# Kernel optimization log

Hardware: AMD Instinct MI355X
Metric: run time of the kernel (lower is better)

## Reference

```python
import jax, jax.numpy as jnp
import numpy as np
from jax import lax

B, H, W = 8, 64, 64
C = 192          # in_channel == out_channel
CI = 384         # inner_channel = int(2.0 * C)


def setup_inputs() -> dict:
    key = jax.random.key(0)
    ks = jax.random.split(key, 8)
    s = 0.02
    return {
        "x": jax.random.normal(ks[0], (B, H, W, C), jnp.float32),
        "Win": jax.random.normal(ks[1], (C, 2 * CI), jnp.float32) * s,
        "conv_w": jax.random.normal(ks[2], (CI, 1, 3, 3), jnp.float32) * s,
        "conv_b": jnp.zeros((CI,), jnp.float32),
        "Wout": jax.random.normal(ks[3], (CI, C), jnp.float32) * s,
        "Wm1": jax.random.normal(ks[4], (C, 4 * C), jnp.float32) * s,
        "bm1": jnp.zeros((4 * C,), jnp.float32),
        "Wm2": jax.random.normal(ks[5], (4 * C, C), jnp.float32) * s,
        "bm2": jnp.zeros((C,), jnp.float32),
    }


def reference(x, Win, conv_w, conv_b, Wout, Wm1, bm1, Wm2, bm2):
    silu = jax.nn.silu
    shortcut = x                                   # [B,H,W,C], norm1 is Identity (norm=None)
    xz = jnp.einsum('bhwc,cd->bhwd', x, Win)       # in_proj (no bias) -> [B,H,W,2*CI]
    x1, z = jnp.split(xz, 2, axis=-1)
    # channel_recover -> [B,CI,H,W], depthwise conv + silu
    xc = jnp.transpose(x1, (0, 3, 1, 2))
    xc = lax.conv_general_dilated(xc, conv_w, (1, 1), 'SAME',
                                  feature_group_count=CI,
                                  dimension_numbers=('NCHW', 'OIHW', 'NCHW'))
    xc = silu(xc + conv_b[None, :, None, None])
    L = H * W
    # cross_scan: K=2 views (row-major and transposed), doubled by flip_scan -> [B,4,CI,L]
    x0 = xc.reshape(B, CI, L)
    xt = jnp.transpose(xc, (0, 1, 3, 2)).reshape(B, CI, L)
    x_cross = jnp.stack([x0, xt], axis=1)
    xs = jnp.concatenate([x_cross, jnp.flip(x_cross, axis=-1)], axis=1)
    out_y = xs  # ssm() is abstract in MBaseBlock -> identity passthrough
    # scan_proj (CrossMerge): undo flips and permutations, sum branches
    inv_y = jnp.flip(out_y[:, 2:4], axis=-1)

    def unperm(v):  # branch scanned in transposed (W,H) order -> back to (H,W)
        return jnp.transpose(v.reshape(B, CI, W, H), (0, 1, 3, 2)).reshape(B, CI, L)

    y = out_y[:, 0] + inv_y[:, 0] + unperm(out_y[:, 1]) + unperm(inv_y[:, 1])
    y = jnp.transpose(y, (0, 2, 1)).reshape(B, H, W, CI)  # norm2 is Identity
    y = y * silu(z)                                       # gate
    out = jnp.einsum('bhwc,cd->bhwd', y, Wout)            # out_proj (no bias)
    out = shortcut + out                                  # dropout/drop_path are Identity
    # dense is Identity (in_channel == out_channel); MLP branch 192->768->192
    h = silu(jnp.einsum('bhwc,cd->bhwd', out, Wm1) + bm1)
    mlp = jnp.einsum('bhwd,dc->bhwc', h, Wm2) + bm2
    return out + mlp
```

## Files before the change

kernel.cpp:

```cpp
#include <hip/hip_runtime.h>
#include <hip/hip_bf16.h>

#define BDIM 8
#define HDIM 64
#define WDIM 64
#define CDIM 192
#define CIDIM 384
#define MTOK (BDIM * HDIM * WDIM)

using bf16 = __hip_bfloat16;
typedef __attribute__((ext_vector_type(8))) short short8;
typedef __attribute__((ext_vector_type(4))) float f32x4;

__device__ __forceinline__ float silu_f(float v) { return v / (1.0f + __expf(-v)); }
__device__ __forceinline__ float bf2f(short s) {
    union { unsigned u; float f; } x; x.u = ((unsigned)(unsigned short)s) << 16; return x.f;
}

__device__ __forceinline__ void gload_lds16(const bf16* g, bf16* l) {
    __builtin_amdgcn_global_load_lds(
        (const __attribute__((address_space(1))) void*)g,
        (__attribute__((address_space(3))) void*)l, 16, 0, 0);
}

#define MFMA16(a, b, c) __builtin_amdgcn_mfma_f32_16x16x32_bf16(a, b, c, 0, 0, 0)

#define NSTRIPE 40
template <int EPI>
__launch_bounds__(256, 2)
__global__ void gemm_k192_p(const bf16* __restrict__ A, const bf16* __restrict__ BT,
                            const float* __restrict__ bias,
                            bf16* __restrict__ outB, bf16* __restrict__ outB2)
{
    __shared__ bf16 As[2][64 * 192];
    __shared__ bf16 Bs[64 * 192];

    const int bid = blockIdx.x;
    const int n   = bid / NSTRIPE;
    const int s   = bid % NSTRIPE;
    const int n0  = n * 64;

    const int tid  = threadIdx.x;
    const int lane = tid & 63;
    const int wv   = tid >> 6;
    const int wm   = wv >> 1;
    const int wn   = wv & 1;

    int soff[6];
    #pragma unroll
    for (int i = 0; i < 6; ++i) {
        const int ci   = wv * 6 + i;
        const int c    = ci * 64 + lane;
        const int row  = c / 24;
        const int slot = c - row * 24;
        soff[i] = row * 192 + (slot ^ (row & 7)) * 8;
    }

    #pragma unroll
    for (int i = 0; i < 6; ++i)
        gload_lds16(BT + (size_t)n0 * 192 + soff[i], &Bs[(wv * 6 + i) * 512]);
    #pragma unroll
    for (int i = 0; i < 6; ++i)
        gload_lds16(A + (size_t)(s * 64) * 192 + soff[i], &As[0][(wv * 6 + i) * 512]);

    const int mloc[2] = { wm * 32 + (lane & 15), wm * 32 + 16 + (lane & 15) };
    const int nloc[2] = { wn * 32 + (lane & 15), wn * 32 + 16 + (lane & 15) };
    const bool isZ = (EPI == 0) && (n0 >= CIDIM);
    bf16* dst        = (EPI == 0) ? (isZ ? outB2 : outB) : outB;
    const int stride = (EPI == 0) ? CIDIM : 768;
    const int col0   = (EPI == 0) ? (isZ ? n0 - CIDIM : n0) : n0;

    int cur = 0;
    for (int mt = s; mt < 512; mt += NSTRIPE) {
        const int nmt = mt + NSTRIPE;
        if (nmt < 512) {
            const bf16* a1 = A + (size_t)(nmt * 64) * 192;
            bf16* db = As[cur ^ 1];
            #pragma unroll
            for (int i = 0; i < 6; ++i)
                gload_lds16(a1 + soff[i], &db[(wv * 6 + i) * 512]);
            asm volatile("s_waitcnt vmcnt(6)" ::: "memory");
        } else {
            asm volatile("s_waitcnt vmcnt(0)" ::: "memory");
        }
        __builtin_amdgcn_sched_barrier(0);
        __builtin_amdgcn_s_barrier();
        __builtin_amdgcn_sched_barrier(0);

        const bf16* la = As[cur];
        f32x4 acc[2][2] = {};
        __builtin_amdgcn_s_setprio(1);
        #pragma unroll
        for (int ks = 0; ks < 6; ++ks) {
            const int t = ks * 4 + (lane >> 4);
            short8 af[2], bfr[2];
            #pragma unroll
            for (int mi = 0; mi < 2; ++mi) {
                const int m = mloc[mi];
                af[mi] = *reinterpret_cast<const short8*>(&la[m * 192 + ((t ^ (m & 7)) << 3)]);
            }
            #pragma unroll
            for (int ni = 0; ni < 2; ++ni) {
                const int nn = nloc[ni];
                bfr[ni] = *reinterpret_cast<const short8*>(&Bs[nn * 192 + ((t ^ (nn & 7)) << 3)]);
            }
            #pragma unroll
            for (int mi = 0; mi < 2; ++mi)
                #pragma unroll
                for (int ni = 0; ni < 2; ++ni)
                    acc[mi][ni] = MFMA16(af[mi], bfr[ni], acc[mi][ni]);
        }
        __builtin_amdgcn_s_setprio(0);

        __builtin_amdgcn_sched_barrier(0);
        __builtin_amdgcn_s_barrier();
        __builtin_amdgcn_sched_barrier(0);

        const int m0   = mt * 64;
        const int rowb = m0 + wm * 32 + (lane >> 4) * 4;
        const int colb = col0 + wn * 32 + (lane & 15);
        #pragma unroll
        for (int mi = 0; mi < 2; ++mi) {
            #pragma unroll
            for (int ni = 0; ni < 2; ++ni) {
                const int c = colb + ni * 16;
                #pragma unroll
                for (int j = 0; j < 4; ++j) {
                    const int row = rowb + mi * 16 + j;
                    float v = acc[mi][ni][j];
                    if constexpr (EPI == 0) {
                        if (isZ) v = 4.0f * silu_f(v);
                    } else {
                        v = silu_f(v + bias[n0 + (c - col0)]);
                    }
                    dst[(size_t)row * stride + c] = __float2bfloat16(v);
                }
            }
        }
        cur ^= 1;
    }
}

__launch_bounds__(256, 4)
__global__ void gemm_g3(const bf16* __restrict__ A, const bf16* __restrict__ BT,
                        const bf16* __restrict__ residB, bf16* __restrict__ outB,
                        int M, int N, int K, int NX)
{
    __shared__ bf16 As[128 * 64];
    __shared__ bf16 Bs[64 * 64];

    const int bid = blockIdx.x;
    const int c8  = bid & 7;
    const int kq  = bid >> 3;
    const int bx  = kq % NX;
    const int by  = (kq / NX) * 8 + c8;
    const int m0  = by * 128;
    const int n0  = bx * 64;

    const int tid  = threadIdx.x;
    const int lane = tid & 63;
    const int wv   = tid >> 6;
    const int wm   = wv >> 1;
    const int wn   = wv & 1;

    const int srow  = lane >> 3;
    const int sslot = lane & 7;

    f32x4 acc[4][2] = {};

    for (int k0 = 0; k0 < K; k0 += 64) {
        #pragma unroll
        for (int i = 0; i < 4; ++i) {
            const int rb = wv * 32 + i * 8;
            const int r  = rb + srow;
            gload_lds16(A + (size_t)(m0 + r) * K + k0 + ((sslot ^ (r & 7)) << 3),
                        &As[rb * 64]);
        }
        #pragma unroll
        for (int i = 0; i < 2; ++i) {
            const int rb = wv * 16 + i * 8;
            const int r  = rb + srow;
            gload_lds16(BT + (size_t)(n0 + r) * K + k0 + ((sslot ^ (r & 7)) << 3),
                        &Bs[rb * 64]);
        }
        __syncthreads();

        #pragma unroll
        for (int kk = 0; kk < 2; ++kk) {
            const int t = kk * 4 + (lane >> 4);
            short8 af[4], bfr[2];
            #pragma unroll
            for (int mi = 0; mi < 4; ++mi) {
                const int m = wm * 64 + mi * 16 + (lane & 15);
                af[mi] = *reinterpret_cast<const short8*>(&As[m * 64 + ((t ^ (m & 7)) << 3)]);
            }
            #pragma unroll
            for (int ni = 0; ni < 2; ++ni) {
                const int n = wn * 32 + ni * 16 + (lane & 15);
                bfr[ni] = *reinterpret_cast<const short8*>(&Bs[n * 64 + ((t ^ (n & 7)) << 3)]);
            }
            #pragma unroll
            for (int mi = 0; mi < 4; ++mi)
                #pragma unroll
                for (int ni = 0; ni < 2; ++ni)
                    acc[mi][ni] = MFMA16(af[mi], bfr[ni], acc[mi][ni]);
        }
        __syncthreads();
    }

    const int colb = n0 + wn * 32 + (lane & 15);
    const int rowb = m0 + wm * 64 + (lane >> 4) * 4;
    #pragma unroll
    for (int mi = 0; mi < 4; ++mi) {
        #pragma unroll
        for (int ni = 0; ni < 2; ++ni) {
            const int c = colb + ni * 16;
            #pragma unroll
            for (int j = 0; j < 4; ++j) {
                const int row = rowb + mi * 16 + j;
                const size_t off = (size_t)row * N + c;
                outB[off] = __float2bfloat16(acc[mi][ni][j] +
                                             bf2f(*(const short*)&residB[off]));
            }
        }
    }
}

#define HSTR 776
__launch_bounds__(256, 2)
__global__ void fused_mlp32(const bf16* __restrict__ ob, const bf16* __restrict__ Wm1F,
                            const bf16* __restrict__ Wm2F, const float* __restrict__ bm1,
                            const float* __restrict__ bm2, float* __restrict__ out)
{
    __shared__ bf16 obs[32 * 192];
    __shared__ bf16 hs[32 * HSTR];

    const int m0   = blockIdx.x * 32;
    const int tid  = threadIdx.x;
    const int lane = tid & 63;
    const int wv   = tid >> 6;
    const int l15  = lane & 15;
    const int l4   = lane >> 4;

    #pragma unroll
    for (int i = 0; i < 3; ++i) {
        const int ci   = wv * 3 + i;
        const int c    = ci * 64 + lane;
        const int row  = c / 24;
        const int slot = c - row * 24;
        gload_lds16(ob + (size_t)(m0 + row) * 192 + ((slot ^ (row & 7)) << 3),
                    &obs[ci * 512]);
    }
    __syncthreads();

    #pragma unroll
    for (int g = 0; g < 3; ++g) {
        f32x4 hacc[2][4] = {};
        #pragma unroll
        for (int ks = 0; ks < 6; ++ks) {
            short8 af[2];
            #pragma unroll
            for (int mi = 0; mi < 2; ++mi) {
                const int r = mi * 16 + l15;
                af[mi] = *reinterpret_cast<const short8*>(
                    &obs[r * 192 + (((ks * 4 + l4) ^ (r & 7)) << 3)]);
            }
            #pragma unroll
            for (int ni = 0; ni < 4; ++ni) {
                const int f = wv * 12 + g * 4 + ni;
                const short8 b = *reinterpret_cast<const short8*>(
                    Wm1F + ((size_t)(f * 6 + ks) * 64 + lane) * 8);
                #pragma unroll
                for (int mi = 0; mi < 2; ++mi)
                    hacc[mi][ni] = MFMA16(af[mi], b, hacc[mi][ni]);
            }
        }
        #pragma unroll
        for (int ni = 0; ni < 4; ++ni) {
            const int col = (wv * 12 + g * 4 + ni) * 16 + l15;
            const float bb = bm1[col];
            #pragma unroll
            for (int mi = 0; mi < 2; ++mi)
                #pragma unroll
                for (int j = 0; j < 4; ++j) {
                    const int r = mi * 16 + l4 * 4 + j;
                    hs[r * HSTR + col] = __float2bfloat16(silu_f(hacc[mi][ni][j] + bb));
                }
        }
    }
    __syncthreads();

    f32x4 facc[2][3] = {};
    for (int ks = 0; ks < 24; ++ks) {
        short8 ha[2];
        #pragma unroll
        for (int mi = 0; mi < 2; ++mi) {
            const int r = mi * 16 + l15;
            ha[mi] = *reinterpret_cast<const short8*>(&hs[r * HSTR + ks * 32 + l4 * 8]);
        }
        #pragma unroll
        for (int ni = 0; ni < 3; ++ni) {
            const int f = wv * 3 + ni;
            const short8 b = *reinterpret_cast<const short8*>(
                Wm2F + ((size_t)(f * 24 + ks) * 64 + lane) * 8);
            #pragma unroll
            for (int mi = 0; mi < 2; ++mi)
                facc[mi][ni] = MFMA16(ha[mi], b, facc[mi][ni]);
        }
    }

    #pragma unroll
    for (int ni = 0; ni < 3; ++ni) {
        const int col = (wv * 3 + ni) * 16 + l15;
        const float b2 = bm2[col];
        #pragma unroll
        for (int mi = 0; mi < 2; ++mi)
            #pragma unroll
            for (int j = 0; j < 4; ++j) {
                const int r  = mi * 16 + l4 * 4 + j;
                const int ch = (col >> 3) ^ (r & 7);
                const float resid = bf2f(*reinterpret_cast<const short*>(
                    &obs[r * 192 + ch * 8 + (col & 7)]));
                out[(size_t)(m0 + r) * 192 + col] = facc[mi][ni][j] + b2 + resid;
            }
    }
}

__launch_bounds__(256)
__global__ void dwconv_gate_v6(const bf16* __restrict__ x1, const bf16* __restrict__ sz,
                               const float* __restrict__ wT, const float* __restrict__ conv_b,
                               bf16* __restrict__ y)
{
    const int bid = blockIdx.x;
    const int swz = (bid & 7) * ((int)gridDim.x >> 3) + (bid >> 3);
    const int f   = swz * 256 + threadIdx.x;
    const int m   = f / 48;
    const int cg  = f - m * 48;
    const int c0  = cg * 8;
    const int h   = (m >> 6) & 63;
    const int w   = m & 63;

    float acc[8];
    {
        const f32x4 ba = *reinterpret_cast<const f32x4*>(&conv_b[c0]);
        const f32x4 bb = *reinterpret_cast<const f32x4*>(&conv_b[c0 + 4]);
        acc[0] = ba[0]; acc[1] = ba[1]; acc[2] = ba[2]; acc[3] = ba[3];
        acc[4] = bb[0]; acc[5] = bb[1]; acc[6] = bb[2]; acc[7] = bb[3];
    }

    #pragma unroll
    for (int r = 0; r < 3; ++r) {
        const int hh = h + r - 1;
        if (hh < 0 || hh >= HDIM) continue;
        #pragma unroll
        for (int dw = 0; dw < 3; ++dw) {
            const int ww = w + dw - 1;
            if (ww < 0 || ww >= WDIM) continue;
            const int mm  = m + (r - 1) * WDIM + (dw - 1);
            const int tap = r * 3 + dw;
            const short8 t = *reinterpret_cast<const short8*>(&x1[(size_t)mm * CIDIM + c0]);
            const f32x4 wa = *reinterpret_cast<const f32x4*>(&wT[tap * CIDIM + c0]);
            const f32x4 wb = *reinterpret_cast<const f32x4*>(&wT[tap * CIDIM + c0 + 4]);
            acc[0] += bf2f(t[0]) * wa[0]; acc[1] += bf2f(t[1]) * wa[1];
            acc[2] += bf2f(t[2]) * wa[2]; acc[3] += bf2f(t[3]) * wa[3];
            acc[4] += bf2f(t[4]) * wb[0]; acc[5] += bf2f(t[5]) * wb[1];
            acc[6] += bf2f(t[6]) * wb[2]; acc[7] += bf2f(t[7]) * wb[3];
        }
    }

    const short8 g = *reinterpret_cast<const short8*>(&sz[(size_t)m * CIDIM + c0]);
    bf16 tmp[8];
    #pragma unroll
    for (int j = 0; j < 8; ++j)
        tmp[j] = __float2bfloat16(silu_f(acc[j]) * bf2f(g[j]));
    *reinterpret_cast<short8*>(&y[(size_t)m * CIDIM + c0]) =
        *reinterpret_cast<const short8*>(tmp);
}

#define SZ_WIN  (192 * 768)
#define SZ_WOUT (384 * 192)
#define SZ_WM1  (192 * 768)
#define SZ_WM2  (768 * 192)
#define SZ_CW   (CIDIM * 9)
#define XCVT    (MTOK * CDIM / 4)
#define SZ_ALL  (XCVT + SZ_WIN + SZ_WOUT + SZ_WM1 + SZ_WM2 + SZ_CW)

__launch_bounds__(256)
__global__ void prep_all(const float* __restrict__ x, const float* __restrict__ Win,
                         const float* __restrict__ Wout, const float* __restrict__ Wm1,
                         const float* __restrict__ Wm2, const float* __restrict__ convw,
                         bf16* __restrict__ xb, bf16* __restrict__ WinT,
                         bf16* __restrict__ WoutT, bf16* __restrict__ Wm1F,
                         bf16* __restrict__ Wm2F, float* __restrict__ wTc)
{
    int idx = blockIdx.x * 256 + threadIdx.x;
    if (idx < XCVT) {
        const int i = idx * 4;
        const float4 v = *reinterpret_cast<const float4*>(&x[i]);
        xb[i + 0] = __float2bfloat16(v.x);
        xb[i + 1] = __float2bfloat16(v.y);
        xb[i + 2] = __float2bfloat16(v.z);
        xb[i + 3] = __float2bfloat16(v.w);
        return;
    }
    idx -= XCVT;
    if (idx < SZ_WIN) {
        const int r = idx / 768, c = idx % 768;
        WinT[(size_t)c * 192 + r] = __float2bfloat16(Win[idx]);
        return;
    }
    idx -= SZ_WIN;
    if (idx < SZ_WOUT) {
        const int r = idx / 192, c = idx % 192;
        WoutT[(size_t)c * 384 + r] = __float2bfloat16(Wout[idx]);
        return;
    }
    idx -= SZ_WOUT;
    if (idx < SZ_WM1) {
        const int f  = idx / 3072;
        const int r1 = idx - f * 3072;
        const int ks = r1 / 512;
        const int r2 = r1 - ks * 512;
        const int l  = r2 >> 3;
        const int e  = r2 & 7;
        const int row = f * 16 + (l & 15);
        const int k   = ks * 32 + (l >> 4) * 8 + e;
        Wm1F[idx] = __float2bfloat16(Wm1[(size_t)k * 768 + row]);
        return;
    }
    idx -= SZ_WM1;
    if (idx < SZ_WM2) {
        const int f  = idx / 12288;
        const int r1 = idx - f * 12288;
        const int ks = r1 / 512;
        const int r2 = r1 - ks * 512;
        const int l  = r2 >> 3;
        const int e  = r2 & 7;
        const int row = f * 16 + (l & 15);
        const int k   = ks * 32 + (l >> 4) * 8 + e;
        Wm2F[idx] = __float2bfloat16(Wm2[(size_t)k * 192 + row]);
        return;
    }
    idx -= SZ_WM2;
    if (idx < SZ_CW) {
        const int ci = idx / 9, t = idx % 9;
        wTc[t * CIDIM + ci] = convw[idx];
    }
}

extern "C" void kernel_launch(void* const* d_in, const int* in_sizes, int n_in,
                              void* d_out, int out_size, void* d_ws, size_t ws_size,
                              hipStream_t stream)
{
    const float* x      = (const float*)d_in[0];
    const float* Win    = (const float*)d_in[1];
    const float* conv_w = (const float*)d_in[2];
    const float* conv_b = (const float*)d_in[3];
    const float* Wout   = (const float*)d_in[4];
    const float* Wm1    = (const float*)d_in[5];
    const float* bm1    = (const float*)d_in[6];
    const float* Wm2    = (const float*)d_in[7];
    const float* bm2    = (const float*)d_in[8];
    float* out = (float*)d_out;

    char* ws = (char*)d_ws;
    size_t o = 0;
    bf16*  xb    = (bf16*)(ws + o); o += (size_t)MTOK * CDIM * 2;
    bf16*  WinT  = (bf16*)(ws + o); o += (size_t)768 * 192 * 2;
    bf16*  WoutT = (bf16*)(ws + o); o += (size_t)192 * 384 * 2;
    bf16*  Wm1F  = (bf16*)(ws + o); o += (size_t)SZ_WM1 * 2;
    bf16*  Wm2F  = (bf16*)(ws + o); o += (size_t)SZ_WM2 * 2;
    float* wTc   = (float*)(ws + o); o += (size_t)9 * CIDIM * 4;
    bf16*  ws_x1 = (bf16*)(ws + o); o += (size_t)MTOK * CIDIM * 2;
    bf16*  ws_sz = (bf16*)(ws + o); o += (size_t)MTOK * CIDIM * 2;
    bf16*  ws_y  = (bf16*)(ws + o); o += (size_t)MTOK * CIDIM * 2;
    bf16*  ws_ob = (bf16*)(ws + o); o += (size_t)MTOK * CDIM * 2;

    prep_all<<<dim3((SZ_ALL + 255) / 256), dim3(256), 0, stream>>>(
        x, Win, Wout, Wm1, Wm2, conv_w, xb, WinT, WoutT, Wm1F, Wm2F, wTc);

    gemm_k192_p<0><<<dim3(12 * NSTRIPE), dim3(256), 0, stream>>>(
        xb, WinT, nullptr, ws_x1, ws_sz);

    dwconv_gate_v6<<<dim3(MTOK * 48 / 256), dim3(256), 0, stream>>>(
        ws_x1, ws_sz, wTc, conv_b, ws_y);

    gemm_g3<<<dim3(3 * 256), dim3(256), 0, stream>>>(
        ws_y, WoutT, xb, ws_ob, MTOK, CDIM, CIDIM, 3);

    fused_mlp32<<<dim3(MTOK / 32), dim3(256), 0, stream>>>(
        ws_ob, Wm1F, Wm2F, bm1, bm2, out);
}
```

Baseline: 117.1 us.

## Chunk MLP hidden dimension to shrink LDS and raise occupancy

The fused MLP kernel now computes the 768-wide hidden activation in three 256-wide chunks and accumulates the second GEMM after each chunk, instead of materialising the full hidden tile in shared memory. This cuts the hidden LDS buffer to about a third, and the launch bound is raised from 2 to 4 blocks per SM to get more resident blocks and better latency hiding. The cost is extra __syncthreads per chunk and a non-unrolled outer loop, and register pressure may limit the occupancy gain.

```diff
diff --git a/kernel.cpp b/kernel.cpp
--- a/kernel.cpp
+++ b/kernel.cpp
@@ -226,14 +226,14 @@
     }
 }
 
-#define HSTR 776
-__launch_bounds__(256, 2)
-__global__ void fused_mlp32(const bf16* __restrict__ ob, const bf16* __restrict__ Wm1F,
-                            const bf16* __restrict__ Wm2F, const float* __restrict__ bm1,
-                            const float* __restrict__ bm2, float* __restrict__ out)
+#define HST2 264
+__launch_bounds__(256, 4)
+__global__ void fused_mlp_kc(const bf16* __restrict__ ob, const bf16* __restrict__ Wm1F,
+                             const bf16* __restrict__ Wm2F, const float* __restrict__ bm1,
+                             const float* __restrict__ bm2, float* __restrict__ out)
 {
     __shared__ bf16 obs[32 * 192];
-    __shared__ bf16 hs[32 * HSTR];
+    __shared__ bf16 hs[32 * HST2];
 
     const int m0   = blockIdx.x * 32;
     const int tid  = threadIdx.x;
@@ -253,8 +253,9 @@
     }
     __syncthreads();
 
-    #pragma unroll
-    for (int g = 0; g < 3; ++g) {
+    f32x4 facc[2][3] = {};
+
+    for (int r3 = 0; r3 < 3; ++r3) {
         f32x4 hacc[2][4] = {};
         #pragma unroll
         for (int ks = 0; ks < 6; ++ks) {
@@ -267,9 +268,9 @@
             }
             #pragma unroll
             for (int ni = 0; ni < 4; ++ni) {
-                const int f = wv * 12 + g * 4 + ni;
+                const int f1 = r3 * 16 + wv * 4 + ni;
                 const short8 b = *reinterpret_cast<const short8*>(
-                    Wm1F + ((size_t)(f * 6 + ks) * 64 + lane) * 8);
+                    Wm1F + ((size_t)(f1 * 6 + ks) * 64 + lane) * 8);
                 #pragma unroll
                 for (int mi = 0; mi < 2; ++mi)
                     hacc[mi][ni] = MFMA16(af[mi], b, hacc[mi][ni]);
@@ -277,36 +278,39 @@
         }
         #pragma unroll
         for (int ni = 0; ni < 4; ++ni) {
-            const int col = (wv * 12 + g * 4 + ni) * 16 + l15;
-            const float bb = bm1[col];
+            const int gcol = (r3 * 16 + wv * 4 + ni) * 16 + l15;
+            const int lc   = (wv * 4 + ni) * 16 + l15;
+            const float bb = bm1[gcol];
             #pragma unroll
             for (int mi = 0; mi < 2; ++mi)
                 #pragma unroll
                 for (int j = 0; j < 4; ++j) {
                     const int r = mi * 16 + l4 * 4 + j;
-                    hs[r * HSTR + col] = __float2bfloat16(silu_f(hacc[mi][ni][j] + bb));
+                    hs[r * HST2 + lc] = __float2bfloat16(silu_f(hacc[mi][ni][j] + bb));
                 }
         }
-    }
-    __syncthreads();
-
-    f32x4 facc[2][3] = {};
-    for (int ks = 0; ks < 24; ++ks) {
-        short8 ha[2];
-        #pragma unroll
-        for (int mi = 0; mi < 2; ++mi) {
-            const int r = mi * 16 + l15;
-            ha[mi] = *reinterpret_cast<const short8*>(&hs[r * HSTR + ks * 32 + l4 * 8]);
-        }
-        #pragma unroll
-        for (int ni = 0; ni < 3; ++ni) {
-            const int f = wv * 3 + ni;
-            const short8 b = *reinterpret_cast<const short8*>(
-                Wm2F + ((size_t)(f * 24 + ks) * 64 + lane) * 8);
-            #pragma unroll
-            for (int mi = 0; mi < 2; ++mi)
-                facc[mi][ni] = MFMA16(ha[mi], b, facc[mi][ni]);
-        }
+        __syncthreads();
+
+        #pragma unroll
+        for (int kk = 0; kk < 8; ++kk) {
+            short8 ha[2];
+            #pragma unroll
+            for (int mi = 0; mi < 2; ++mi) {
+                const int r = mi * 16 + l15;
+                ha[mi] = *reinterpret_cast<const short8*>(&hs[r * HST2 + kk * 32 + l4 * 8]);
+            }
+            #pragma unroll
+            for (int ni = 0; ni < 3; ++ni) {
+                const int f2  = wv * 3 + ni;
+                const int gks = r3 * 8 + kk;
+                const short8 b = *reinterpret_cast<const short8*>(
+                    Wm2F + ((size_t)(f2 * 24 + gks) * 64 + lane) * 8);
+                #pragma unroll
+                for (int mi = 0; mi < 2; ++mi)
+                    facc[mi][ni] = MFMA16(ha[mi], b, facc[mi][ni]);
+            }
+        }
+        __syncthreads();
     }
 
     #pragma unroll
@@ -488,6 +492,6 @@
     gemm_g3<<<dim3(3 * 256), dim3(256), 0, stream>>>(
         ws_y, WoutT, xb, ws_ob, MTOK, CDIM, CIDIM, 3);
 
-    fused_mlp32<<<dim3(MTOK / 32), dim3(256), 0, stream>>>(
+    fused_mlp_kc<<<dim3(MTOK / 32), dim3(256), 0, stream>>>(
         ws_ob, Wm1F, Wm2F, bm1, bm2, out);
 }
```

New measurement: 125.0 us. 1.07x slower.
